# Kernel optimization log

Measured on AMD Instinct MI355X. Metric: run time of the kernel, lower is better.

## Reference

```python
import jax, jax.numpy as jnp
import numpy as np

N = 10000      # nodes per graph-batch
E = 160000     # edges
G = 128        # number of graphs (segments)


def gcn_conv(x, edge_index, W, b, n):
    """PyG GCNConv with normalize=True, add_self_loops=True.
    x: [n, in], W: [in, out], b: [out], edge_index: [2, e]."""
    loops = jnp.arange(n, dtype=edge_index.dtype)
    src = jnp.concatenate([edge_index[0], loops])
    dst = jnp.concatenate([edge_index[1], loops])
    deg = jnp.zeros((n,), x.dtype).at[dst].add(1.0)          # in-degree incl. self-loops
    dinv = jnp.where(deg > 0, jax.lax.rsqrt(deg), 0.0)
    norm = dinv[src] * dinv[dst]                              # [e+n]
    h = x @ W                                                 # dense transform first
    out = jax.ops.segment_sum(norm[:, None] * h[src], dst, num_segments=n)
    return out + b


def global_max_pool(z, batch, g):
    p = jax.ops.segment_max(z, batch, num_segments=g)
    return jnp.where(jnp.isneginf(p), 0.0, p)  # guard empty segments


def setup_inputs() -> dict:
    key = jax.random.key(0)
    ks = jax.random.split(key, 24)

    def w(k, i, o):
        return (jax.random.normal(k, (i, o), jnp.float32) / np.sqrt(i)).astype(jnp.float32)

    inp = {
        "x_s": jax.random.normal(ks[0], (N, 128), jnp.float32),
        "x_t": jax.random.normal(ks[1], (N, 128), jnp.float32),
        "edge_index_s": jax.random.randint(ks[2], (2, E), 0, N, dtype=jnp.int32),
        "edge_index_t": jax.random.randint(ks[3], (2, E), 0, N, dtype=jnp.int32),
        "xs_batch": jnp.sort(jax.random.randint(ks[4], (N,), 0, G, dtype=jnp.int32)),
        "xt_batch": jnp.sort(jax.random.randint(ks[5], (N,), 0, G, dtype=jnp.int32)),
        # encoder GCNConvs (128 -> 512)
        "W_enc1": w(ks[6], 128, 512), "b_enc1": jnp.zeros((512,), jnp.float32),
        "W_enc2": w(ks[7], 128, 512), "b_enc2": jnp.zeros((512,), jnp.float32),
        # branch-1 GCNConvs
        "W_r1g1": w(ks[8], 512, 1024), "b_r1g1": jnp.zeros((1024,), jnp.float32),
        "W_r1g2": w(ks[9], 1024, 2048), "b_r1g2": jnp.zeros((2048,), jnp.float32),
        # branch-2 GCNConvs
        "W_r2g1": w(ks[10], 512, 1024), "b_r2g1": jnp.zeros((1024,), jnp.float32),
        "W_r2g2": w(ks[11], 1024, 2048), "b_r2g2": jnp.zeros((2048,), jnp.float32),
        # MLP head
        "W_l1": w(ks[12], 2048, 1024), "b_l1": jnp.zeros((1024,), jnp.float32),
        "W_l2": w(ks[13], 1024, 1317), "b_l2": jnp.zeros((1317,), jnp.float32),
    }
    return inp


def reference(x_s, x_t, W_enc1, b_enc1, W_enc2, b_enc2,
              W_r1g1, b_r1g1, W_r1g2, b_r1g2,
              W_r2g1, b_r2g1, W_r2g2, b_r2g2,
              W_l1, b_l1, W_l2, b_l2,
              edge_index_s, edge_index_t, xs_batch, xt_batch):
    # branch 1 (source graphs)
    enc_r1 = gcn_conv(x_s, edge_index_s, W_enc1, b_enc1, N)
    z_r1 = jax.nn.relu(gcn_conv(enc_r1, edge_index_s, W_r1g1, b_r1g1, N))
    z_r1 = jax.nn.relu(gcn_conv(z_r1, edge_index_s, W_r1g2, b_r1g2, N))
    # branch 2 (target graphs)
    enc_r2 = gcn_conv(x_t, edge_index_t, W_enc2, b_enc2, N)
    z_r2 = jax.nn.relu(gcn_conv(enc_r2, edge_index_t, W_r2g1, b_r2g1, N))
    z_r2 = jax.nn.relu(gcn_conv(z_r2, edge_index_t, W_r2g2, b_r2g2, N))
    # global max pool per graph, then MLP head
    z = global_max_pool(z_r1, xs_batch, G) + global_max_pool(z_r2, xt_batch, G)  # [G, 2048]
    z = jax.nn.relu(z @ W_l1 + b_l1)
    z = z @ W_l2 + b_l2                                                          # [G, 1317]
    return (z, jax.nn.sigmoid(z))
```

## Files before the change

kernel.cpp:

```cpp
#include <hip/hip_runtime.h>
#include <cstdint>
#include <cstddef>


#define NN 10000
#define NNP 10112
#define MT 20224
#define NE 160000
#define NG 128

typedef short bf16x8 __attribute__((ext_vector_type(8)));
typedef float f32x4 __attribute__((ext_vector_type(4)));

__device__ __forceinline__ unsigned short f2bf(float x) {
  unsigned u = __float_as_uint(x);
  u += 0x7FFFu + ((u >> 16) & 1u);
  return (unsigned short)(u >> 16);
}
__device__ __forceinline__ float bf2f(unsigned short h) {
  return __uint_as_float(((unsigned)h) << 16);
}
__device__ __forceinline__ void fma4(float4& d, float s, const float4& u) {
  d.x = fmaf(s, u.x, d.x);
  d.y = fmaf(s, u.y, d.y);
  d.z = fmaf(s, u.z, d.z);
  d.w = fmaf(s, u.w, d.w);
}

#define GLOAD_LDS16(gp, lp)                                                  \
  __builtin_amdgcn_global_load_lds(                                          \
      (const __attribute__((address_space(1))) void*)(gp),                   \
      (__attribute__((address_space(3))) void*)(lp), 16, 0, 0)


__global__ void k_fill_i32(int* __restrict__ p, int v, int n) {
  int i = blockIdx.x * blockDim.x + threadIdx.x;
  if (i < n) p[i] = v;
}

__global__ void k_count2(const int* __restrict__ eis, const int* __restrict__ eit,
                         int* __restrict__ cnt) {
  int i = blockIdx.x * blockDim.x + threadIdx.x;
  if (i >= 2 * NE) return;
  int d;
  if (i < NE) d = eis[NE + i];
  else        d = eit[NE + (i - NE)] + NNP;
  atomicAdd(&cnt[d], 1);
}

__global__ void k_scan(const int* __restrict__ cnt, int* __restrict__ row_ptr,
                       int* __restrict__ cursor, float* __restrict__ dinv,
                       const int* __restrict__ bs, const int* __restrict__ bt,
                       int* __restrict__ seg) {
  __shared__ int part[256];
  __shared__ int partex[257];
  int t = threadIdx.x;
  const int n = MT;
  const int CH = (n + 255) / 256;
  int base = t * CH;
  int s = 0;
  for (int i = 0; i < CH; ++i) {
    int idx = base + i;
    if (idx < n) s += cnt[idx];
  }
  part[t] = s;
  __syncthreads();
  if (t == 0) {
    int acc = 0;
    for (int i = 0; i < 256; ++i) { partex[i] = acc; acc += part[i]; }
    partex[256] = acc;
  }
  __syncthreads();
  int acc = partex[t];
  for (int i = 0; i < CH; ++i) {
    int idx = base + i;
    if (idx < n) {
      row_ptr[idx] = acc;
      cursor[idx]  = acc;
      dinv[idx] = rsqrtf((float)cnt[idx] + 1.0f);
      acc += cnt[idx];
    }
  }
  if (t == 255) row_ptr[n] = partex[256];
  if (t <= NG) {
    int lo = 0, hi = NN;
    while (lo < hi) {
      int mid = (lo + hi) >> 1;
      if (bs[mid] < t) lo = mid + 1;
      else hi = mid;
    }
    seg[t] = lo;
    lo = 0; hi = NN;
    while (lo < hi) {
      int mid = (lo + hi) >> 1;
      if (bt[mid] < t) lo = mid + 1;
      else hi = mid;
    }
    seg[(NG + 1) + t] = lo;
  }
}

__global__ void k_scatter2(const int* __restrict__ eis, const int* __restrict__ eit,
                           const float* __restrict__ dinv, int* __restrict__ cursor,
                           int2* __restrict__ csr) {
  int i = blockIdx.x * blockDim.x + threadIdx.x;
  if (i >= 2 * NE) return;
  int s, d;
  if (i < NE) { s = eis[i]; d = eis[NE + i]; }
  else { int j = i - NE; s = eit[j] + NNP; d = eit[NE + j] + NNP; }
  int pos = atomicAdd(&cursor[d], 1);
  float w = dinv[s] * dinv[d];
  csr[pos] = make_int2(s, __float_as_int(w));
}

template <int F4TOT, bool DUAL>
__global__ __launch_bounds__(256) void k_agg_c(
    const float* __restrict__ in0, const float* __restrict__ in1,
    unsigned short* __restrict__ Ah, unsigned short* __restrict__ Al,
    const int* __restrict__ row_ptr, const int2* __restrict__ csr,
    const float* __restrict__ dinv) {
  int t = threadIdx.x;
  int node = blockIdx.x * 32 + (t >> 3);
  int f4 = blockIdx.y * 8 + (t & 7);
  size_t o = (size_t)node * F4TOT + f4;
  ushort4* oh = (ushort4*)Ah + o;
  ushort4* ol = (ushort4*)Al + o;
  int local = (node < NNP) ? node : (node - NNP);
  if (local >= NN) {
    *oh = make_ushort4(0, 0, 0, 0);
    *ol = make_ushort4(0, 0, 0, 0);
    return;
  }
  const float4* i0 = (const float4*)in0;
  const float4* i1 = (const float4*)in1;

  auto rowp = [&](int g) -> const float4* {
    if (DUAL)
      return (g < NNP) ? (i0 + (size_t)g * F4TOT)
                       : (i1 + (size_t)(g - NNP) * F4TOT);
    return i0 + (size_t)g * F4TOT;
  };

  float di = dinv[node];
  float sw = di * di;
  float4 v = rowp(node)[f4];
  float4 acc;
  acc.x = sw * v.x; acc.y = sw * v.y; acc.z = sw * v.z; acc.w = sw * v.w;

  int e0 = row_ptr[node], e1 = row_ptr[node + 1];
  int e = e0;
  for (; e + 4 <= e1; e += 4) {
    int2 p0 = csr[e], p1 = csr[e + 1], p2 = csr[e + 2], p3 = csr[e + 3];
    float4 u0 = rowp(p0.x)[f4];
    float4 u1 = rowp(p1.x)[f4];
    float4 u2 = rowp(p2.x)[f4];
    float4 u3 = rowp(p3.x)[f4];
    fma4(acc, __int_as_float(p0.y), u0);
    fma4(acc, __int_as_float(p1.y), u1);
    fma4(acc, __int_as_float(p2.y), u2);
    fma4(acc, __int_as_float(p3.y), u3);
  }
  for (; e < e1; ++e) {
    int2 p = csr[e];
    float4 u = rowp(p.x)[f4];
    fma4(acc, __int_as_float(p.y), u);
  }

  ushort4 h, l;
  h.x = f2bf(acc.x); l.x = f2bf(acc.x - bf2f(h.x));
  h.y = f2bf(acc.y); l.y = f2bf(acc.y - bf2f(h.y));
  h.z = f2bf(acc.z); l.z = f2bf(acc.z - bf2f(h.z));
  h.w = f2bf(acc.w); l.w = f2bf(acc.w - bf2f(h.w));
  *oh = h;
  *ol = l;
}

__global__ __launch_bounds__(256) void k_wsplit2(
    const float* __restrict__ W0, unsigned short* __restrict__ H0,
    unsigned short* __restrict__ L0,
    const float* __restrict__ W1, unsigned short* __restrict__ H1,
    unsigned short* __restrict__ L1, int K, int N) {
  const float* W = blockIdx.z ? W1 : W0;
  unsigned short* Ht = blockIdx.z ? H1 : H0;
  unsigned short* Lt = blockIdx.z ? L1 : L0;
  __shared__ float tile[32][33];
  int nb = blockIdx.x * 32, kb = blockIdx.y * 32;
  int tx = threadIdx.x & 31, ty = threadIdx.x >> 5;
#pragma unroll
  for (int r = ty; r < 32; r += 8)
    tile[r][tx] = W[(size_t)(kb + r) * N + nb + tx];
  __syncthreads();
#pragma unroll
  for (int r = ty; r < 32; r += 8) {
    float x = tile[tx][r];
    unsigned short h = f2bf(x);
    unsigned short lo = f2bf(x - bf2f(h));
    size_t o = (size_t)(nb + r) * K + kb + tx;
    Ht[o] = h;
    Lt[o] = lo;
  }
}

template <bool RELU, int GX>
__global__ __launch_bounds__(256) void k_mgemm(
    const unsigned short* __restrict__ Ah, const unsigned short* __restrict__ Al,
    const unsigned short* __restrict__ Bh_a, const unsigned short* __restrict__ Bl_a,
    const unsigned short* __restrict__ Bh_b, const unsigned short* __restrict__ Bl_b,
    const float* __restrict__ bias_a, const float* __restrict__ bias_b,
    float* __restrict__ C, int N, int K, int AOFF) {
  __shared__ char smem[65536];
  const int t = threadIdx.x;
  const int w = t >> 6, l = t & 63;

  const int bid = blockIdx.x;
  int bn_, bm_;
  if constexpr (GX == 16) { bn_ = 2 * (bid & 7) + ((bid >> 3) & 1); bm_ = bid >> 4; }
  else if constexpr (GX == 8) { bn_ = bid & 7; bm_ = bid >> 3; }
  else { bn_ = bid & (GX - 1); bm_ = bid / GX; }
  const int bm = bm_ * 128, bn = bn_ * 128;
  const int arow = bm + AOFF;
  const bool sec = arow >= NNP;
  const unsigned short* Bh = sec ? Bh_b : Bh_a;
  const unsigned short* Bl = sec ? Bl_b : Bl_a;
  const float* bias = sec ? bias_b : bias_a;

  const int wr = w >> 1, wc = w & 1;

  f32x4 acc[4][4] = {};

  const unsigned short* g0 = (w == 0) ? Ah : (w == 1) ? Al : (w == 2) ? Bh : Bl;
  const int rb = (w < 2) ? arow : bn;
  const unsigned short* gbase = g0 + (size_t)(rb + (l & 15)) * K + ((l >> 4) * 8);
  const int sdoff = w * 8192 + l * 16;
  const int saoff = wr * 4096 + l * 16;
  const int sboff = 16384 + wc * 4096 + l * 16;

  const int nt = K >> 5;

#define STAGE(kt, b)                                                         \
  {                                                                          \
    const unsigned short* gk = gbase + ((kt) << 5);                          \
    char* sd = smem + (b)*32768 + sdoff;                                     \
    _Pragma("unroll") for (int s = 0; s < 8; ++s)                            \
        GLOAD_LDS16(gk + (size_t)s * 16 * K, sd + s * 1024);                 \
  }

  STAGE(0, 0)

  for (int kt = 0; kt < nt; ++kt) {
    const int cur = kt & 1;
    if (kt + 1 < nt) {
      STAGE(kt + 1, cur ^ 1)
      asm volatile("s_waitcnt vmcnt(8)" ::: "memory");
    } else {
      asm volatile("s_waitcnt vmcnt(0)" ::: "memory");
    }
    __builtin_amdgcn_sched_barrier(0);
    __builtin_amdgcn_s_barrier();

    const char* sA = smem + cur * 32768 + saoff;
    const char* sB = smem + cur * 32768 + sboff;
    bf16x8 a[4][2], b[4][2];
#pragma unroll
    for (int i = 0; i < 4; ++i) {
      a[i][0] = *(const bf16x8*)(sA + i * 1024);
      a[i][1] = *(const bf16x8*)(sA + 8192 + i * 1024);
    }
#pragma unroll
    for (int j = 0; j < 4; ++j) {
      b[j][0] = *(const bf16x8*)(sB + j * 1024);
      b[j][1] = *(const bf16x8*)(sB + 8192 + j * 1024);
    }
    asm volatile("s_waitcnt lgkmcnt(0)" ::: "memory");
    __builtin_amdgcn_sched_barrier(0);
    __builtin_amdgcn_s_barrier();

    __builtin_amdgcn_s_setprio(1);
#pragma unroll
    for (int i = 0; i < 4; ++i)
#pragma unroll
      for (int j = 0; j < 4; ++j) {
        acc[i][j] = __builtin_amdgcn_mfma_f32_16x16x32_bf16(a[i][0], b[j][0], acc[i][j], 0, 0, 0);
        acc[i][j] = __builtin_amdgcn_mfma_f32_16x16x32_bf16(a[i][0], b[j][1], acc[i][j], 0, 0, 0);
        acc[i][j] = __builtin_amdgcn_mfma_f32_16x16x32_bf16(a[i][1], b[j][0], acc[i][j], 0, 0, 0);
      }
    __builtin_amdgcn_s_setprio(0);
  }
#undef STAGE

  const int r0 = bm + wr * 64 + ((l >> 4) << 2);
  const int c0 = bn + wc * 64 + (l & 15);
#pragma unroll
  for (int j = 0; j < 4; ++j) {
    const int col = c0 + j * 16;
    const float bv = bias[col];
#pragma unroll
    for (int i = 0; i < 4; ++i) {
      const int row = r0 + i * 16;
#pragma unroll
      for (int r = 0; r < 4; ++r) {
        float v = acc[i][j][r] + bv;
        if (RELU) v = fmaxf(v, 0.f);
        C[(size_t)(row + r) * N + col] = v;
      }
    }
  }
}

__global__ __launch_bounds__(256) void k_gemm_sk(
    const float* __restrict__ A, const float* __restrict__ A2,
    const float* __restrict__ B,
    float* __restrict__ PART, int M, int N, int K, int KS) {
  __shared__ float As[32][64];
  __shared__ float Bs[32][64];

  int t = threadIdx.x;
  int tx = t & 15, ty = t >> 4;
  int bm = blockIdx.y * 64, bn = blockIdx.x * 64;
  int kbeg = blockIdx.z * KS, kend = kbeg + KS;

  float acc[4][4] = {};

  int arow0 = t >> 3;
  int ak4 = (t & 7) * 4;
  int brow0 = t >> 4;
  int bn4 = (t & 15) * 4;
  const bool n4al = (N & 3) == 0;

  for (int k0 = kbeg; k0 < kend; k0 += 32) {
#pragma unroll
    for (int c = 0; c < 2; ++c) {
      int row = arow0 + c * 32;
      int gr = bm + row;
      float4 v = make_float4(0.f, 0.f, 0.f, 0.f);
      if (gr < M) {
        v = *(const float4*)&A[(size_t)gr * K + k0 + ak4];
        if (A2) {
          float4 v2 = *(const float4*)&A2[(size_t)gr * K + k0 + ak4];
          v.x += v2.x; v.y += v2.y; v.z += v2.z; v.w += v2.w;
        }
      }
      As[ak4 + 0][row] = v.x;
      As[ak4 + 1][row] = v.y;
      As[ak4 + 2][row] = v.z;
      As[ak4 + 3][row] = v.w;
    }
#pragma unroll
    for (int c = 0; c < 2; ++c) {
      int row = brow0 + c * 16;
      int gc = bn + bn4;
      const float* bp = &B[(size_t)(k0 + row) * N + gc];
      float4 v;
      if (n4al && gc + 3 < N) {
        v = *(const float4*)bp;
      } else {
        v = make_float4(0.f, 0.f, 0.f, 0.f);
        if (gc < N) v.x = bp[0];
        if (gc + 1 < N) v.y = bp[1];
        if (gc + 2 < N) v.z = bp[2];
        if (gc + 3 < N) v.w = bp[3];
      }
      *(float4*)&Bs[row][bn4] = v;
    }
    __syncthreads();

#pragma unroll
    for (int kk = 0; kk < 32; ++kk) {
      float4 a = *(const float4*)&As[kk][ty * 4];
      float4 b = *(const float4*)&Bs[kk][tx * 4];
      float av[4] = {a.x, a.y, a.z, a.w};
      float bv[4] = {b.x, b.y, b.z, b.w};
#pragma unroll
      for (int i = 0; i < 4; ++i)
#pragma unroll
        for (int j = 0; j < 4; ++j)
          acc[i][j] = fmaf(av[i], bv[j], acc[i][j]);
    }
    __syncthreads();
  }

  float* P = PART + (size_t)blockIdx.z * M * N;
  int r0 = bm + ty * 4, c0 = bn + tx * 4;
#pragma unroll
  for (int i = 0; i < 4; ++i) {
    int r = r0 + i;
    if (r < M) {
#pragma unroll
      for (int j = 0; j < 4; ++j) {
        int c = c0 + j;
        if (c < N) P[(size_t)r * N + c] = acc[i][j];
      }
    }
  }
}

template <bool SIG>
__global__ void k_reduce(const float* __restrict__ PART,
                         const float* __restrict__ bias,
                         float* __restrict__ C, float* __restrict__ C2,
                         int MN, int N, int SK) {
  int i = blockIdx.x * blockDim.x + threadIdx.x;
  if (i >= MN) return;
  float s = 0.f;
  for (int z = 0; z < SK; ++z) s += PART[(size_t)z * MN + i];
  s += bias[i % N];
  if (SIG) {
    C[i] = s;
    C2[i] = 1.0f / (1.0f + __expf(-s));
  } else {
    C[i] = fmaxf(s, 0.f);
  }
}


__global__ void k_pool(const float* __restrict__ act, const int* __restrict__ segp,
                       float* __restrict__ P, int F4) {
  int g = blockIdx.x;
  int f4 = blockIdx.y * blockDim.x + threadIdx.x;
  if (f4 >= F4) return;
  const float4* a4 = (const float4*)act;
  int i0 = segp[g], i1 = segp[g + 1];
  float4 m = make_float4(0.f, 0.f, 0.f, 0.f);
  for (int i = i0; i < i1; ++i) {
    float4 u = a4[(size_t)i * F4 + f4];
    m.x = fmaxf(m.x, u.x);
    m.y = fmaxf(m.y, u.y);
    m.z = fmaxf(m.z, u.z);
    m.w = fmaxf(m.w, u.w);
  }
  ((float4*)P)[(size_t)g * F4 + f4] = m;
}


extern "C" void kernel_launch(void* const* d_in, const int* in_sizes, int n_in,
                              void* d_out, int out_size, void* d_ws, size_t ws_size,
                              hipStream_t stream) {
  const float* x_s = (const float*)d_in[0];
  const float* x_t = (const float*)d_in[1];
  const int* ei_s = (const int*)d_in[2];
  const int* ei_t = (const int*)d_in[3];
  const int* xs_batch = (const int*)d_in[4];
  const int* xt_batch = (const int*)d_in[5];
  const float* W_enc1 = (const float*)d_in[6];
  const float* b_enc1 = (const float*)d_in[7];
  const float* W_enc2 = (const float*)d_in[8];
  const float* b_enc2 = (const float*)d_in[9];
  const float* W_r1g1 = (const float*)d_in[10];
  const float* b_r1g1 = (const float*)d_in[11];
  const float* W_r1g2 = (const float*)d_in[12];
  const float* b_r1g2 = (const float*)d_in[13];
  const float* W_r2g1 = (const float*)d_in[14];
  const float* b_r2g1 = (const float*)d_in[15];
  const float* W_r2g2 = (const float*)d_in[16];
  const float* b_r2g2 = (const float*)d_in[17];
  const float* W_l1 = (const float*)d_in[18];
  const float* b_l1 = (const float*)d_in[19];
  const float* W_l2 = (const float*)d_in[20];
  const float* b_l2 = (const float*)d_in[21];

  float* out = (float*)d_out;

  char* ws = (char*)d_ws;
  size_t off = 0;
  auto carve = [&](size_t bytes) {
    char* p = ws + off;
    off = (off + bytes + 255) & ~(size_t)255;
    return p;
  };
  float* ACT = (float*)carve((size_t)MT * 1024 * 4);
  float* ACT3 = ACT;
  unsigned short* Ah = (unsigned short*)carve((size_t)MT * 1024 * 2);
  unsigned short* Al = (unsigned short*)carve((size_t)MT * 1024 * 2);
  unsigned short* W1h_a = (unsigned short*)carve((size_t)512 * 128 * 2);
  unsigned short* W1l_a = (unsigned short*)carve((size_t)512 * 128 * 2);
  unsigned short* W1h_b = (unsigned short*)carve((size_t)512 * 128 * 2);
  unsigned short* W1l_b = (unsigned short*)carve((size_t)512 * 128 * 2);
  unsigned short* W2h_a = (unsigned short*)carve((size_t)1024 * 512 * 2);
  unsigned short* W2l_a = (unsigned short*)carve((size_t)1024 * 512 * 2);
  unsigned short* W2h_b = (unsigned short*)carve((size_t)1024 * 512 * 2);
  unsigned short* W2l_b = (unsigned short*)carve((size_t)1024 * 512 * 2);
  unsigned short* W3h_a = (unsigned short*)carve((size_t)2048 * 1024 * 2);
  unsigned short* W3l_a = (unsigned short*)carve((size_t)2048 * 1024 * 2);
  unsigned short* W3h_b = (unsigned short*)carve((size_t)2048 * 1024 * 2);
  unsigned short* W3l_b = (unsigned short*)carve((size_t)2048 * 1024 * 2);
  float* P2   = (float*)carve((size_t)2 * NG * 2048 * 4);
  float* ZZ   = (float*)carve((size_t)NG * 1024 * 4);
  float* PART = (float*)carve((size_t)16 * NG * 1024 * 4);
  float* dinv = (float*)carve((size_t)MT * 4);
  int* cnt     = (int*)carve((size_t)MT * 4);
  int* row_ptr = (int*)carve((size_t)(MT + 1) * 4);
  int* cursor  = (int*)carve((size_t)MT * 4);
  int2* csr    = (int2*)carve((size_t)2 * NE * 8);
  int* seg     = (int*)carve((size_t)2 * (NG + 1) * 4);
  (void)ws_size; (void)n_in; (void)in_sizes; (void)out_size;

  k_wsplit2<<<dim3(512 / 32, 128 / 32, 2), 256, 0, stream>>>(
      W_enc1, W1h_a, W1l_a, W_enc2, W1h_b, W1l_b, 128, 512);
  k_wsplit2<<<dim3(1024 / 32, 512 / 32, 2), 256, 0, stream>>>(
      W_r1g1, W2h_a, W2l_a, W_r2g1, W2h_b, W2l_b, 512, 1024);
  k_wsplit2<<<dim3(2048 / 32, 1024 / 32, 2), 256, 0, stream>>>(
      W_r1g2, W3h_a, W3l_a, W_r2g2, W3h_b, W3l_b, 1024, 2048);

  k_fill_i32<<<(MT + 255) / 256, 256, 0, stream>>>(cnt, 0, MT);
  k_count2<<<(2 * NE + 255) / 256, 256, 0, stream>>>(ei_s, ei_t, cnt);
  k_scan<<<1, 256, 0, stream>>>(cnt, row_ptr, cursor, dinv, xs_batch, xt_batch, seg);
  k_scatter2<<<(2 * NE + 255) / 256, 256, 0, stream>>>(ei_s, ei_t, dinv, cursor, csr);

  k_agg_c<32, true><<<dim3(MT / 32, 4), 256, 0, stream>>>(
      x_s, x_t, Ah, Al, row_ptr, csr, dinv);
  k_mgemm<false, 4><<<4 * (MT / 128), 256, 0, stream>>>(
      Ah, Al, W1h_a, W1l_a, W1h_b, W1l_b, b_enc1, b_enc2, ACT, 512, 128, 0);

  k_agg_c<128, false><<<dim3(MT / 32, 16), 256, 0, stream>>>(
      ACT, nullptr, Ah, Al, row_ptr, csr, dinv);
  k_mgemm<true, 8><<<8 * (MT / 128), 256, 0, stream>>>(
      Ah, Al, W2h_a, W2l_a, W2h_b, W2l_b, b_r1g1, b_r2g1, ACT, 1024, 512, 0);

  k_agg_c<256, false><<<dim3(MT / 32, 32), 256, 0, stream>>>(
      ACT, nullptr, Ah, Al, row_ptr, csr, dinv);
  k_mgemm<true, 16><<<16 * (NNP / 128), 256, 0, stream>>>(
      Ah, Al, W3h_a, W3l_a, W3h_b, W3l_b, b_r1g2, b_r2g2, ACT3, 2048, 1024, 0);
  k_pool<<<dim3(NG, 2), 256, 0, stream>>>(ACT3, seg, P2, 512);
  k_mgemm<true, 16><<<16 * (NNP / 128), 256, 0, stream>>>(
      Ah, Al, W3h_a, W3l_a, W3h_b, W3l_b, b_r1g2, b_r2g2, ACT3, 2048, 1024, NNP);
  k_pool<<<dim3(NG, 2), 256, 0, stream>>>(ACT3, seg + (NG + 1),
                                          P2 + (size_t)NG * 2048, 512);

  k_gemm_sk<<<dim3(1024 / 64, 2, 16), 256, 0, stream>>>(
      P2, P2 + (size_t)NG * 2048, W_l1, PART, NG, 1024, 2048, 128);
  k_reduce<false><<<(NG * 1024 + 255) / 256, 256, 0, stream>>>(
      PART, b_l1, ZZ, nullptr, NG * 1024, 1024, 16);

  const int OUTN = 1317;
  k_gemm_sk<<<dim3((OUTN + 63) / 64, 2, 8), 256, 0, stream>>>(
      ZZ, nullptr, W_l2, PART, NG, OUTN, 1024, 128);
  k_reduce<true><<<(NG * OUTN + 255) / 256, 256, 0, stream>>>(
      PART, b_l2, out, out + (size_t)NG * OUTN, NG * OUTN, OUTN, 8);
}
```

Before: 842.6 us.

## Remap aggregation blocks per XCD and shrink CSR to source indices

The aggregation kernel now uses a 1D grid whose block index is remapped so that each XCD (bid&7) handles one feature chunk across node blocks. The intent is to keep the gathered feature columns resident in that XCD's L2. The CSR now stores only source indices, and edge weights are recomputed from dinv at aggregation time, which halves CSR traffic and removes the dinv gather from scatter. This adds an extra dinv gather per edge in each aggregation. The fill kernel is also replaced by hipMemsetAsync.

```diff
diff --git a/kernel.cpp b/kernel.cpp
--- a/kernel.cpp
+++ b/kernel.cpp
@@ -6,6 +6,7 @@
 #define NN 10000
 #define NNP 10112
 #define MT 20224
+#define NB 632
 #define NE 160000
 #define NG 128
 
@@ -32,11 +33,6 @@
       (const __attribute__((address_space(1))) void*)(gp),                   \
       (__attribute__((address_space(3))) void*)(lp), 16, 0, 0)
 
-
-__global__ void k_fill_i32(int* __restrict__ p, int v, int n) {
-  int i = blockIdx.x * blockDim.x + threadIdx.x;
-  if (i < n) p[i] = v;
-}
 
 __global__ void k_count2(const int* __restrict__ eis, const int* __restrict__ eit,
                          int* __restrict__ cnt) {
@@ -101,27 +97,39 @@
 }
 
 __global__ void k_scatter2(const int* __restrict__ eis, const int* __restrict__ eit,
-                           const float* __restrict__ dinv, int* __restrict__ cursor,
-                           int2* __restrict__ csr) {
+                           int* __restrict__ cursor, int* __restrict__ csr_src) {
   int i = blockIdx.x * blockDim.x + threadIdx.x;
   if (i >= 2 * NE) return;
   int s, d;
   if (i < NE) { s = eis[i]; d = eis[NE + i]; }
   else { int j = i - NE; s = eit[j] + NNP; d = eit[NE + j] + NNP; }
   int pos = atomicAdd(&cursor[d], 1);
-  float w = dinv[s] * dinv[d];
-  csr[pos] = make_int2(s, __float_as_int(w));
-}
-
-template <int F4TOT, bool DUAL>
-__global__ __launch_bounds__(256) void k_agg_c(
+  csr_src[pos] = s;
+}
+
+template <int NCH, bool DUAL>
+__global__ __launch_bounds__(256) void k_agg_x(
     const float* __restrict__ in0, const float* __restrict__ in1,
     unsigned short* __restrict__ Ah, unsigned short* __restrict__ Al,
-    const int* __restrict__ row_ptr, const int2* __restrict__ csr,
+    const int* __restrict__ row_ptr, const int* __restrict__ csr_src,
     const float* __restrict__ dinv) {
-  int t = threadIdx.x;
-  int node = blockIdx.x * 32 + (t >> 3);
-  int f4 = blockIdx.y * 8 + (t & 7);
+  constexpr int F4TOT = NCH * 8;
+  const int bid = blockIdx.x;
+  const int xcd = bid & 7;
+  const int seq = bid >> 3;
+  int chunk, nodeblk;
+  if constexpr (NCH >= 8) {
+    int phase = seq / NB;
+    nodeblk = seq - phase * NB;
+    chunk = phase * 8 + xcd;
+  } else {
+    chunk = xcd >> 1;
+    nodeblk = (seq << 1) | (xcd & 1);
+  }
+  const int t = threadIdx.x;
+  const int node = nodeblk * 32 + (t >> 3);
+  const int f4 = chunk * 8 + (t & 7);
+
   size_t o = (size_t)node * F4TOT + f4;
   ushort4* oh = (ushort4*)Ah + o;
   ushort4* ol = (ushort4*)Al + o;
@@ -133,7 +141,6 @@
   }
   const float4* i0 = (const float4*)in0;
   const float4* i1 = (const float4*)in1;
-
   auto rowp = [&](int g) -> const float4* {
     if (DUAL)
       return (g < NNP) ? (i0 + (size_t)g * F4TOT)
@@ -147,23 +154,26 @@
   float4 acc;
   acc.x = sw * v.x; acc.y = sw * v.y; acc.z = sw * v.z; acc.w = sw * v.w;
 
-  int e0 = row_ptr[node], e1 = row_ptr[node + 1];
+  const int e0 = row_ptr[node], e1 = row_ptr[node + 1];
   int e = e0;
   for (; e + 4 <= e1; e += 4) {
-    int2 p0 = csr[e], p1 = csr[e + 1], p2 = csr[e + 2], p3 = csr[e + 3];
-    float4 u0 = rowp(p0.x)[f4];
-    float4 u1 = rowp(p1.x)[f4];
-    float4 u2 = rowp(p2.x)[f4];
-    float4 u3 = rowp(p3.x)[f4];
-    fma4(acc, __int_as_float(p0.y), u0);
-    fma4(acc, __int_as_float(p1.y), u1);
-    fma4(acc, __int_as_float(p2.y), u2);
-    fma4(acc, __int_as_float(p3.y), u3);
+    int s0 = csr_src[e], s1 = csr_src[e + 1];
+    int s2 = csr_src[e + 2], s3 = csr_src[e + 3];
+    float4 u0 = rowp(s0)[f4];
+    float4 u1 = rowp(s1)[f4];
+    float4 u2 = rowp(s2)[f4];
+    float4 u3 = rowp(s3)[f4];
+    float w0 = dinv[s0] * di, w1 = dinv[s1] * di;
+    float w2 = dinv[s2] * di, w3 = dinv[s3] * di;
+    fma4(acc, w0, u0);
+    fma4(acc, w1, u1);
+    fma4(acc, w2, u2);
+    fma4(acc, w3, u3);
   }
   for (; e < e1; ++e) {
-    int2 p = csr[e];
-    float4 u = rowp(p.x)[f4];
-    fma4(acc, __int_as_float(p.y), u);
+    int s = csr_src[e];
+    float4 u = rowp(s)[f4];
+    fma4(acc, dinv[s] * di, u);
   }
 
   ushort4 h, l;
@@ -490,7 +500,7 @@
   int* cnt     = (int*)carve((size_t)MT * 4);
   int* row_ptr = (int*)carve((size_t)(MT + 1) * 4);
   int* cursor  = (int*)carve((size_t)MT * 4);
-  int2* csr    = (int2*)carve((size_t)2 * NE * 8);
+  int* csr_src = (int*)carve((size_t)2 * NE * 4);
   int* seg     = (int*)carve((size_t)2 * (NG + 1) * 4);
   (void)ws_size; (void)n_in; (void)in_sizes; (void)out_size;
 
@@ -501,23 +511,23 @@
   k_wsplit2<<<dim3(2048 / 32, 1024 / 32, 2), 256, 0, stream>>>(
       W_r1g2, W3h_a, W3l_a, W_r2g2, W3h_b, W3l_b, 1024, 2048);
 
-  k_fill_i32<<<(MT + 255) / 256, 256, 0, stream>>>(cnt, 0, MT);
+  hipMemsetAsync(cnt, 0, (size_t)MT * 4, stream);
   k_count2<<<(2 * NE + 255) / 256, 256, 0, stream>>>(ei_s, ei_t, cnt);
   k_scan<<<1, 256, 0, stream>>>(cnt, row_ptr, cursor, dinv, xs_batch, xt_batch, seg);
-  k_scatter2<<<(2 * NE + 255) / 256, 256, 0, stream>>>(ei_s, ei_t, dinv, cursor, csr);
-
-  k_agg_c<32, true><<<dim3(MT / 32, 4), 256, 0, stream>>>(
-      x_s, x_t, Ah, Al, row_ptr, csr, dinv);
+  k_scatter2<<<(2 * NE + 255) / 256, 256, 0, stream>>>(ei_s, ei_t, cursor, csr_src);
+
+  k_agg_x<4, true><<<NB * 4, 256, 0, stream>>>(
+      x_s, x_t, Ah, Al, row_ptr, csr_src, dinv);
   k_mgemm<false, 4><<<4 * (MT / 128), 256, 0, stream>>>(
       Ah, Al, W1h_a, W1l_a, W1h_b, W1l_b, b_enc1, b_enc2, ACT, 512, 128, 0);
 
-  k_agg_c<128, false><<<dim3(MT / 32, 16), 256, 0, stream>>>(
-      ACT, nullptr, Ah, Al, row_ptr, csr, dinv);
+  k_agg_x<16, false><<<NB * 16, 256, 0, stream>>>(
+      ACT, nullptr, Ah, Al, row_ptr, csr_src, dinv);
   k_mgemm<true, 8><<<8 * (MT / 128), 256, 0, stream>>>(
       Ah, Al, W2h_a, W2l_a, W2h_b, W2l_b, b_r1g1, b_r2g1, ACT, 1024, 512, 0);
 
-  k_agg_c<256, false><<<dim3(MT / 32, 32), 256, 0, stream>>>(
-      ACT, nullptr, Ah, Al, row_ptr, csr, dinv);
+  k_agg_x<32, false><<<NB * 32, 256, 0, stream>>>(
+      ACT, nullptr, Ah, Al, row_ptr, csr_src, dinv);
   k_mgemm<true, 16><<<16 * (NNP / 128), 256, 0, stream>>>(
       Ah, Al, W3h_a, W3l_a, W3h_b, W3l_b, b_r1g2, b_r2g2, ACT3, 2048, 1024, 0);
   k_pool<<<dim3(NG, 2), 256, 0, stream>>>(ACT3, seg, P2, 512);
```

Measured after the change: 835.2 us. Within noise of the previous version (-0.9%).
